# Optimization experiments

Hardware: AMD Instinct MI355X
Metric: run time of the kernel (lower is better)

Reference implementation:

```python
import jax, jax.numpy as jnp
import numpy as np
from jax import lax

T, B, D_IN, H, D_OUT = 512, 64, 256, 512, 256


def _lstm_scan(xs, h0, c0, Wih, Whh, b):
    """Standard LSTM over time. xs: [T,B,Din]; returns (hs [T,B,H], hT, cT).
    Gate order i,f,g,o (PyTorch convention)."""
    def step(carry, x_t):
        h, c = carry
        gates = x_t @ Wih.T + h @ Whh.T + b            # [B, 4H]
        i, f, g, o = jnp.split(gates, 4, axis=-1)
        i = jax.nn.sigmoid(i)
        f = jax.nn.sigmoid(f)
        g = jnp.tanh(g)
        o = jax.nn.sigmoid(o)
        c = f * c + i * g
        h = o * jnp.tanh(c)
        return (h, c), h
    (hT, cT), hs = lax.scan(step, (h0, c0), xs)
    return hs, hT, cT


def setup_inputs() -> dict:
    key = jax.random.key(0)
    ks = jax.random.split(key, 10)
    s = 0.05
    return {
        "x": jax.random.normal(ks[0], (T, B, D_IN), jnp.float32),
        "target": jax.random.uniform(ks[1], (T, B, D_OUT), jnp.float32),
        "hidden_state": jnp.zeros((1, B, H), jnp.float32),
        "cell_state": jnp.zeros((1, B, H), jnp.float32),
        "enc_Wih": jax.random.normal(ks[2], (4 * H, D_IN), jnp.float32) * s,
        "enc_Whh": jax.random.normal(ks[3], (4 * H, H), jnp.float32) * s,
        "enc_b": jax.random.normal(ks[4], (4 * H,), jnp.float32) * s,
        "dec_Wih": jax.random.normal(ks[5], (4 * H, D_OUT), jnp.float32) * s,
        "dec_Whh": jax.random.normal(ks[6], (4 * H, H), jnp.float32) * s,
        "dec_b": jax.random.normal(ks[7], (4 * H,), jnp.float32) * s,
        "fc_W": jax.random.normal(ks[8], (D_OUT, H), jnp.float32) * s,
        "fc_b": jax.random.normal(ks[9], (D_OUT,), jnp.float32) * s,
    }


def reference(x, target, hidden_state, cell_state,
              enc_Wih, enc_Whh, enc_b, dec_Wih, dec_Whh, dec_b, fc_W, fc_b):
    # Encoder: consume x, keep final (h, c).
    _, h, c = _lstm_scan(x, hidden_state[0], cell_state[0], enc_Wih, enc_Whh, enc_b)
    # Decoder with teacher_forcing = 1.0: input at step t is target[t-1],
    # step 0 input is zeros (matches torch code's initial x = zeros).
    dec_in = jnp.concatenate([jnp.zeros((1,) + target.shape[1:], target.dtype),
                              target[:-1]], axis=0)          # [T, B, D_OUT]
    hs, _, _ = _lstm_scan(dec_in, h, c, dec_Wih, dec_Whh, dec_b)  # [T, B, H]
    logits = hs @ fc_W.T + fc_b                                   # [T, B, D_OUT]
    return jax.nn.softmax(logits, axis=-1)
```

## Files before the change

### kernel.cpp

```cpp
#include <hip/hip_runtime.h>
#include <math.h>

#define TT 512
#define BB 64
#define DIN 256
#define HH 512
#define DOUT 256

#define RSU 388
#define RSH 776

#define W_HI_OFF 0
#define W_LO_OFF 12416
#define A_HI_OFF 24832
#define A_LO_OFF 31040
#define P_OFF    37248
#define B_OFF    38528
#define C_OFF    38560
#define HST_HI   38688
#define HST_LO   38752
#define SMEM_U32 38816
#define SMEM_BYTES (SMEM_U32*4)

#define FCS 516

typedef _Float16 f16x8 __attribute__((ext_vector_type(8)));
typedef float    f32x4 __attribute__((ext_vector_type(4)));
typedef unsigned u32x4 __attribute__((ext_vector_type(4)));

union H16 { _Float16 f; unsigned short u; };
__device__ __forceinline__ unsigned short f16bits(_Float16 h) { H16 t; t.f = h; return t.u; }

__device__ __forceinline__ void pack2(float x, float y, unsigned& hi, unsigned& lo) {
    _Float16 hx = (_Float16)x, hy = (_Float16)y;
    _Float16 lx = (_Float16)((x - (float)hx) * 2048.0f);
    _Float16 ly = (_Float16)((y - (float)hy) * 2048.0f);
    hi = (unsigned)f16bits(hx) | ((unsigned)f16bits(hy) << 16);
    lo = (unsigned)f16bits(lx) | ((unsigned)f16bits(ly) << 16);
}

__device__ __forceinline__ u32x4 ld16_cohere(const void* p) {
    u32x4 v;
    asm volatile("global_load_dwordx4 %0, %1, off sc0 sc1"
                 : "=&v"(v) : "v"(p) : "memory");
    return v;
}
__device__ __forceinline__ void st16_cohere(void* p, u32x4 v) {
    asm volatile("global_store_dwordx4 %0, %1, off sc0 sc1"
                 :: "v"(p), "v"(v) : "memory");
}

__device__ __forceinline__ void load_w_f16(unsigned* __restrict__ sm32, float* __restrict__ b_l,
                                           const float* __restrict__ Whh,
                                           const float* __restrict__ Wih,
                                           const float* __restrict__ bias,
                                           int u0, int tid) {
    for (int r = 0; r < 48; ++r) {
        int id = tid + 256*r;
        int cc = id / 384;
        int jj = id - cc*384;
        int C  = (cc >> 3)*HH + u0 + (cc & 7);
        float2 v;
        if (jj < 256) v = ((const float2*)(Whh + (size_t)C*HH))[jj];
        else          v = ((const float2*)(Wih + (size_t)C*DIN))[jj - 256];
        unsigned hi, lo;
        pack2(v.x, v.y, hi, lo);
        sm32[W_HI_OFF + cc*RSU + jj] = hi;
        sm32[W_LO_OFF + cc*RSU + jj] = lo;
    }
    if (tid < 32) {
        int C = (tid >> 3)*HH + u0 + (tid & 7);
        b_l[tid] = bias[C];
    }
}

__device__ __forceinline__ void stage_x_f16(unsigned* __restrict__ sm32,
                                            const float* __restrict__ src, int tid) {
    for (int r = 0; r < 4; ++r) {
        int idx4 = tid + 256*r;
        int b = idx4 >> 6, j4 = idx4 & 63;
        float4 v = ((const float4*)(src + (size_t)b*DIN))[j4];
        unsigned h0, l0, h1, l1;
        pack2(v.x, v.y, h0, l0);
        pack2(v.z, v.w, h1, l1);
        int o = b*RSU + 256 + 2*j4;
        sm32[A_HI_OFF + o]     = h0;
        sm32[A_HI_OFF + o + 1] = h1;
        sm32[A_LO_OFF + o]     = l0;
        sm32[A_LO_OFF + o + 1] = l1;
    }
}

__device__ __forceinline__ void stage_x_zero_f16(unsigned* __restrict__ sm32, int tid) {
    for (int r = 0; r < 4; ++r) {
        int idx4 = tid + 256*r;
        int b = idx4 >> 6, j4 = idx4 & 63;
        int o = b*RSU + 256 + 2*j4;
        sm32[A_HI_OFF + o]     = 0u;
        sm32[A_HI_OFF + o + 1] = 0u;
        sm32[A_LO_OFF + o]     = 0u;
        sm32[A_LO_OFF + o + 1] = 0u;
    }
}

__global__ __launch_bounds__(256, 1)
void lstm_persist(const float* __restrict__ x, const float* __restrict__ target,
                  const float* __restrict__ h0, const float* __restrict__ c0,
                  const float* __restrict__ eWih, const float* __restrict__ eWhh,
                  const float* __restrict__ eb,
                  const float* __restrict__ dWih, const float* __restrict__ dWhh,
                  const float* __restrict__ db,
                  float* __restrict__ hs,
                  unsigned short* __restrict__ hbh,
                  unsigned short* __restrict__ hbl,
                  unsigned* __restrict__ bar)
{
    extern __shared__ unsigned sm32[];
    float* p_l = (float*)(sm32 + P_OFF);
    float* b_l = (float*)(sm32 + B_OFF);
    float* c_l = (float*)(sm32 + C_OFF);
    unsigned* hst_hi = sm32 + HST_HI;
    unsigned* hst_lo = sm32 + HST_LO;

    const int tid = (int)threadIdx.x;
    const int xcd = (int)(blockIdx.x & 7);
    const int ib  = xcd >> 1;
    const int sub = xcd & 1;
    const int ij  = (int)(blockIdx.x >> 3) | (sub << 5);
    const int b0  = ib * 16;
    const int u0  = ij * 8;
    unsigned* gflags = bar + ib*64;

    load_w_f16(sm32, b_l, eWhh, eWih, eb, u0, tid);
    if (tid < 128) {
        int b = tid >> 3, u = tid & 7;
        c_l[tid] = c0[(size_t)(b0 + b)*HH + u0 + u];
    }
    stage_x_f16(sm32, x + (size_t)b0*DIN, tid);
    for (int r = 0; r < 8; ++r) {
        int idx4 = tid + 256*r;
        int b = idx4 >> 7, j4 = idx4 & 127;
        float4 v = ((const float4*)(h0 + (size_t)(b0 + b)*HH))[j4];
        unsigned h0p, l0p, h1p, l1p;
        pack2(v.x, v.y, h0p, l0p);
        pack2(v.z, v.w, h1p, l1p);
        int o = b*RSU + 2*j4;
        sm32[A_HI_OFF + o]     = h0p;
        sm32[A_HI_OFF + o + 1] = h1p;
        sm32[A_LO_OFF + o]     = l0p;
        sm32[A_LO_OFF + o + 1] = l1p;
    }
    __syncthreads();

    const int lane = tid & 63;
    const int wid  = tid >> 6;
    const int m    = lane & 15;
    const int q    = lane >> 4;
    const int ct   = wid & 1;
    const int kh   = wid >> 1;

    const _Float16* aH = (const _Float16*)(sm32 + A_HI_OFF);
    const _Float16* aL = (const _Float16*)(sm32 + A_LO_OFF);
    const _Float16* wH = (const _Float16*)(sm32 + W_HI_OFF);
    const _Float16* wL = (const _Float16*)(sm32 + W_LO_OFF);
    const int aoff = m*RSH + q*8;
    const int woff = (ct*16 + m)*RSH + q*8;

    for (int s = 0; s < 1024; ++s) {
        f32x4 Chh = {0.f, 0.f, 0.f, 0.f};
        f32x4 Chl = {0.f, 0.f, 0.f, 0.f};
        f32x4 Clh = {0.f, 0.f, 0.f, 0.f};
        {
            const int ks0 = kh * 12;
            #pragma unroll
            for (int i = 0; i < 12; ++i) {
                const int o = (ks0 + i) * 32;
                f16x8 ah = *(const f16x8*)(aH + aoff + o);
                f16x8 al = *(const f16x8*)(aL + aoff + o);
                f16x8 wh = *(const f16x8*)(wH + woff + o);
                f16x8 wl = *(const f16x8*)(wL + woff + o);
                Chh = __builtin_amdgcn_mfma_f32_16x16x32_f16(ah, wh, Chh, 0, 0, 0);
                Chl = __builtin_amdgcn_mfma_f32_16x16x32_f16(ah, wl, Chl, 0, 0, 0);
                Clh = __builtin_amdgcn_mfma_f32_16x16x32_f16(al, wh, Clh, 0, 0, 0);
            }
        }
        {
            float4 C;
            const float sc = 1.0f / 2048.0f;
            C.x = Chh[0] + (Chl[0] + Clh[0]) * sc;
            C.y = Chh[1] + (Chl[1] + Clh[1]) * sc;
            C.z = Chh[2] + (Chl[2] + Clh[2]) * sc;
            C.w = Chh[3] + (Chl[3] + Clh[3]) * sc;
            *(float4*)(p_l + (ct*2 + kh)*320 + m*20 + q*4) = C;
        }
        __syncthreads();

        float hval = 0.f;
        if (tid < 128) {
            int b = tid >> 3, u = tid & 7;
            float gi = p_l[      u*20 + b] + p_l[320 +      u*20 + b] + b_l[u];
            float gf = p_l[(8+u)*20 + b] + p_l[320 + (8+u)*20 + b] + b_l[8 + u];
            float gg = p_l[640 +   u*20 + b] + p_l[960 +      u*20 + b] + b_l[16 + u];
            float go = p_l[640 + (8+u)*20 + b] + p_l[960 + (8+u)*20 + b] + b_l[24 + u];
            float ii = 1.f / (1.f + expf(-gi));
            float ff = 1.f / (1.f + expf(-gf));
            float g2 = tanhf(gg);
            float oo = 1.f / (1.f + expf(-go));
            float c  = ff * c_l[tid] + ii * g2;
            c_l[tid] = c;
            hval = oo * tanhf(c);
            _Float16 hh = (_Float16)hval;
            _Float16 hl = (_Float16)((hval - (float)hh) * 2048.0f);
            ((unsigned short*)hst_hi)[tid] = f16bits(hh);
            ((unsigned short*)hst_lo)[tid] = f16bits(hl);
        }
        __syncthreads();

        if (tid < 64) {
            if (tid < 32) {
                int b    = tid & 15;
                int isLo = tid >> 4;
                u32x4 v = *(const u32x4*)((isLo ? hst_lo : hst_hi) + b*4);
                unsigned short* base = isLo ? hbl : hbh;
                st16_cohere(base + ((size_t)(((s & 1) ^ 1))*BB + b0 + b)*HH + u0, v);
            }
            asm volatile("s_waitcnt vmcnt(0)" ::: "memory");
            if (tid == 0)
                __hip_atomic_store(&gflags[ij], (unsigned)(s + 1),
                                   __ATOMIC_RELAXED, __HIP_MEMORY_SCOPE_AGENT);
        }

        if (s >= 512 && tid < 128) {
            int b = tid >> 3, u = tid & 7;
            hs[((size_t)(s - 512)*BB + (b0 + b))*HH + (u0 + u)] = hval;
        }
        if (s == 511) load_w_f16(sm32, b_l, dWhh, dWih, db, u0, tid);
        {
            int ns = s + 1;
            if (ns < 1024) {
                if (ns == 512)       stage_x_zero_f16(sm32, tid);
                else if (ns < 512)   stage_x_f16(sm32, x + ((size_t)ns*BB + b0)*DIN, tid);
                else                 stage_x_f16(sm32, target + ((size_t)(ns - 513)*BB + b0)*DOUT, tid);
            }
        }

        if (s < 1023) {
            if (tid < 64) {
                while (true) {
                    unsigned v = __hip_atomic_load(&gflags[tid], __ATOMIC_RELAXED,
                                                   __HIP_MEMORY_SCOPE_AGENT);
                    if (__ballot(v >= (unsigned)(s + 1)) == ~0ull) break;
                    __builtin_amdgcn_s_sleep(1);
                }
            }
            __syncthreads();
            const unsigned short* srcH = hbh + (size_t)((s + 1) & 1)*BB*HH + (size_t)b0*HH;
            const unsigned short* srcL = hbl + (size_t)((s + 1) & 1)*BB*HH + (size_t)b0*HH;
            u32x4 h0v = ld16_cohere((const u32x4*)srcH + tid);
            u32x4 h1v = ld16_cohere((const u32x4*)srcH + tid + 256);
            u32x4 h2v = ld16_cohere((const u32x4*)srcH + tid + 512);
            u32x4 h3v = ld16_cohere((const u32x4*)srcH + tid + 768);
            u32x4 l0v = ld16_cohere((const u32x4*)srcL + tid);
            u32x4 l1v = ld16_cohere((const u32x4*)srcL + tid + 256);
            u32x4 l2v = ld16_cohere((const u32x4*)srcL + tid + 512);
            u32x4 l3v = ld16_cohere((const u32x4*)srcL + tid + 768);
            asm volatile("s_waitcnt vmcnt(0)"
                         : "+v"(h0v), "+v"(h1v), "+v"(h2v), "+v"(h3v),
                           "+v"(l0v), "+v"(l1v), "+v"(l2v), "+v"(l3v) :: "memory");
            {
                int idx, b, j0;
                idx = tid;       b = idx >> 6; j0 = (idx & 63)*4;
                *(u32x4*)(sm32 + A_HI_OFF + b*RSU + j0) = h0v;
                *(u32x4*)(sm32 + A_LO_OFF + b*RSU + j0) = l0v;
                idx = tid + 256; b = idx >> 6; j0 = (idx & 63)*4;
                *(u32x4*)(sm32 + A_HI_OFF + b*RSU + j0) = h1v;
                *(u32x4*)(sm32 + A_LO_OFF + b*RSU + j0) = l1v;
                idx = tid + 512; b = idx >> 6; j0 = (idx & 63)*4;
                *(u32x4*)(sm32 + A_HI_OFF + b*RSU + j0) = h2v;
                *(u32x4*)(sm32 + A_LO_OFF + b*RSU + j0) = l2v;
                idx = tid + 768; b = idx >> 6; j0 = (idx & 63)*4;
                *(u32x4*)(sm32 + A_HI_OFF + b*RSU + j0) = h3v;
                *(u32x4*)(sm32 + A_LO_OFF + b*RSU + j0) = l3v;
            }
        }
        __syncthreads();
    }
}

__global__ __launch_bounds__(256, 1)
void fc_kernel(const float* __restrict__ hs, const float* __restrict__ W,
               const float* __restrict__ bias, float* __restrict__ out)
{
    extern __shared__ float sm[];
    float* hs_l = sm;
    float* w_l  = sm + 16*FCS;

    const int tid = (int)threadIdx.x;
    const int rb = (int)(blockIdx.x >> 3);
    const int cb = (int)(blockIdx.x & 7);

    for (int r = 0; r < 8; ++r) {
        int id = tid + 256*r;
        int b = id >> 7, j = id & 127;
        float4 v = ((const float4*)(hs + (size_t)(rb*16 + b)*HH))[j];
        *(float4*)(hs_l + b*FCS + 4*j) = v;
    }
    for (int r = 0; r < 16; ++r) {
        int id = tid + 256*r;
        int c = id >> 7, j = id & 127;
        float4 v = ((const float4*)(W + (size_t)(cb*32 + c)*HH))[j];
        *(float4*)(w_l + c*FCS + 4*j) = v;
    }
    __syncthreads();

    const int kc = tid & 7, bt = (tid >> 3) & 3, ct = tid >> 5;
    float acc[4][4] = {};
    const float* ap = hs_l + (bt*4)*FCS + 4*kc;
    const float* wp = w_l  + (ct*4)*FCS + 4*kc;
    #pragma unroll 4
    for (int i = 0; i < 16; ++i) {
        float4 av[4], wv[4];
        #pragma unroll
        for (int q = 0; q < 4; ++q) av[q] = *(const float4*)(ap + q*FCS + 32*i);
        #pragma unroll
        for (int q = 0; q < 4; ++q) wv[q] = *(const float4*)(wp + q*FCS + 32*i);
        #pragma unroll
        for (int b2 = 0; b2 < 4; ++b2)
            #pragma unroll
            for (int c2 = 0; c2 < 4; ++c2)
                acc[b2][c2] += av[b2].x*wv[c2].x + av[b2].y*wv[c2].y
                             + av[b2].z*wv[c2].z + av[b2].w*wv[c2].w;
    }
    #pragma unroll
    for (int b2 = 0; b2 < 4; ++b2)
        #pragma unroll
        for (int c2 = 0; c2 < 4; ++c2) {
            float v = acc[b2][c2];
            v += __shfl_xor(v, 1, 64);
            v += __shfl_xor(v, 2, 64);
            v += __shfl_xor(v, 4, 64);
            acc[b2][c2] = v;
        }
    if (kc == 0) {
        #pragma unroll
        for (int b2 = 0; b2 < 4; ++b2)
            #pragma unroll
            for (int c2 = 0; c2 < 4; ++c2) {
                int row = rb*16 + bt*4 + b2;
                int col = cb*32 + ct*4 + c2;
                out[(size_t)row*DOUT + col] = acc[b2][c2] + bias[col];
            }
    }
}

__global__ __launch_bounds__(256, 1)
void softmax_kernel(float* __restrict__ out)
{
    int row  = (int)blockIdx.x * 4 + ((int)threadIdx.x >> 6);
    int lane = (int)threadIdx.x & 63;
    float4 v = ((const float4*)(out + (size_t)row*DOUT))[lane];
    float m = fmaxf(fmaxf(v.x, v.y), fmaxf(v.z, v.w));
    #pragma unroll
    for (int d = 1; d < 64; d <<= 1) m = fmaxf(m, __shfl_xor(m, d, 64));
    float ex = expf(v.x - m), ey = expf(v.y - m), ez = expf(v.z - m), ew = expf(v.w - m);
    float ssum = ex + ey + ez + ew;
    #pragma unroll
    for (int d = 1; d < 64; d <<= 1) ssum += __shfl_xor(ssum, d, 64);
    float inv = 1.f / ssum;
    float4 o = make_float4(ex*inv, ey*inv, ez*inv, ew*inv);
    ((float4*)(out + (size_t)row*DOUT))[lane] = o;
}

__global__ void init_kernel(unsigned* __restrict__ bar)
{
    bar[threadIdx.x] = 0u;
}

extern "C" void kernel_launch(void* const* d_in, const int* in_sizes, int n_in,
                              void* d_out, int out_size, void* d_ws, size_t ws_size,
                              hipStream_t stream) {
    (void)in_sizes; (void)n_in; (void)out_size; (void)ws_size;
    const float* x      = (const float*)d_in[0];
    const float* target = (const float*)d_in[1];
    const float* h0     = (const float*)d_in[2];
    const float* c0     = (const float*)d_in[3];
    const float* eWih   = (const float*)d_in[4];
    const float* eWhh   = (const float*)d_in[5];
    const float* eb     = (const float*)d_in[6];
    const float* dWih   = (const float*)d_in[7];
    const float* dWhh   = (const float*)d_in[8];
    const float* db     = (const float*)d_in[9];
    const float* fcW    = (const float*)d_in[10];
    const float* fcb    = (const float*)d_in[11];
    float* out = (float*)d_out;

    unsigned* bar = (unsigned*)d_ws;
    float* hs = (float*)d_ws + 1024;
    unsigned short* hbh = (unsigned short*)(hs + (size_t)TT*BB*HH);
    unsigned short* hbl = hbh + (size_t)2*BB*HH;

    init_kernel<<<dim3(1), dim3(1024), 0, stream>>>(bar);

    lstm_persist<<<dim3(256), dim3(256), SMEM_BYTES, stream>>>(
        x, target, h0, c0, eWih, eWhh, eb, dWih, dWhh, db, hs, hbh, hbl, bar);

    size_t lds_fc = (size_t)(48*FCS) * sizeof(float);
    fc_kernel<<<dim3(16384), dim3(256), lds_fc, stream>>>(hs, fcW, fcb, out);

    softmax_kernel<<<dim3(8192), dim3(256), 0, stream>>>(out);
}
```

Before: 4.658 ms.

## Precompute input projection off critical path and reorder hidden-state exchange layout

The input-side MFMA products (x·Wih) for the next step are now computed right after the current step finishes, before the barrier wait. This takes them off the serialized critical path, so the in-loop matmul only covers the recurrent h·Whh part. The global hidden-state exchange buffer is laid out per batch-group in a contiguous block, so each block writes one contiguous chunk and reads contiguously. Staging of the next input and writing of hs are moved onto otherwise idle threads. These changes add accumulator registers and make the staging and indexing logic more intricate.

```diff
diff --git a/kernel.cpp b/kernel.cpp
--- a/kernel.cpp
+++ b/kernel.cpp
@@ -30,6 +30,7 @@
 
 union H16 { _Float16 f; unsigned short u; };
 __device__ __forceinline__ unsigned short f16bits(_Float16 h) { H16 t; t.f = h; return t.u; }
+__device__ __forceinline__ float f16val(unsigned short b) { H16 t; t.u = b; return (float)t.f; }
 
 __device__ __forceinline__ void pack2(float x, float y, unsigned& hi, unsigned& lo) {
     _Float16 hx = (_Float16)x, hy = (_Float16)y;
@@ -71,35 +72,6 @@
     if (tid < 32) {
         int C = (tid >> 3)*HH + u0 + (tid & 7);
         b_l[tid] = bias[C];
-    }
-}
-
-__device__ __forceinline__ void stage_x_f16(unsigned* __restrict__ sm32,
-                                            const float* __restrict__ src, int tid) {
-    for (int r = 0; r < 4; ++r) {
-        int idx4 = tid + 256*r;
-        int b = idx4 >> 6, j4 = idx4 & 63;
-        float4 v = ((const float4*)(src + (size_t)b*DIN))[j4];
-        unsigned h0, l0, h1, l1;
-        pack2(v.x, v.y, h0, l0);
-        pack2(v.z, v.w, h1, l1);
-        int o = b*RSU + 256 + 2*j4;
-        sm32[A_HI_OFF + o]     = h0;
-        sm32[A_HI_OFF + o + 1] = h1;
-        sm32[A_LO_OFF + o]     = l0;
-        sm32[A_LO_OFF + o + 1] = l1;
-    }
-}
-
-__device__ __forceinline__ void stage_x_zero_f16(unsigned* __restrict__ sm32, int tid) {
-    for (int r = 0; r < 4; ++r) {
-        int idx4 = tid + 256*r;
-        int b = idx4 >> 6, j4 = idx4 & 63;
-        int o = b*RSU + 256 + 2*j4;
-        sm32[A_HI_OFF + o]     = 0u;
-        sm32[A_HI_OFF + o + 1] = 0u;
-        sm32[A_LO_OFF + o]     = 0u;
-        sm32[A_LO_OFF + o + 1] = 0u;
     }
 }
 
@@ -136,19 +108,31 @@
         int b = tid >> 3, u = tid & 7;
         c_l[tid] = c0[(size_t)(b0 + b)*HH + u0 + u];
     }
-    stage_x_f16(sm32, x + (size_t)b0*DIN, tid);
+    for (int r = 0; r < 4; ++r) {
+        int idx4 = tid + 256*r;
+        int b = idx4 >> 6, j4 = idx4 & 63;
+        float4 v = ((const float4*)(x + ((size_t)b0 + b)*DIN))[j4];
+        unsigned hp0, lp0, hp1, lp1;
+        pack2(v.x, v.y, hp0, lp0);
+        pack2(v.z, v.w, hp1, lp1);
+        int o = b*RSU + 256 + 2*j4;
+        sm32[A_HI_OFF + o]     = hp0;
+        sm32[A_HI_OFF + o + 1] = hp1;
+        sm32[A_LO_OFF + o]     = lp0;
+        sm32[A_LO_OFF + o + 1] = lp1;
+    }
     for (int r = 0; r < 8; ++r) {
         int idx4 = tid + 256*r;
         int b = idx4 >> 7, j4 = idx4 & 127;
         float4 v = ((const float4*)(h0 + (size_t)(b0 + b)*HH))[j4];
-        unsigned h0p, l0p, h1p, l1p;
-        pack2(v.x, v.y, h0p, l0p);
-        pack2(v.z, v.w, h1p, l1p);
+        unsigned hp0, lp0, hp1, lp1;
+        pack2(v.x, v.y, hp0, lp0);
+        pack2(v.z, v.w, hp1, lp1);
         int o = b*RSU + 2*j4;
-        sm32[A_HI_OFF + o]     = h0p;
-        sm32[A_HI_OFF + o + 1] = h1p;
-        sm32[A_LO_OFF + o]     = l0p;
-        sm32[A_LO_OFF + o + 1] = l1p;
+        sm32[A_HI_OFF + o]     = hp0;
+        sm32[A_HI_OFF + o + 1] = hp1;
+        sm32[A_LO_OFF + o]     = lp0;
+        sm32[A_LO_OFF + o + 1] = lp1;
     }
     __syncthreads();
 
@@ -166,15 +150,71 @@
     const int aoff = m*RSH + q*8;
     const int woff = (ct*16 + m)*RSH + q*8;
 
+    f32x4 Ahh = {0.f,0.f,0.f,0.f}, Ahl = {0.f,0.f,0.f,0.f}, Alh = {0.f,0.f,0.f,0.f};
+    {
+        const int xs0 = 16 + kh*4;
+        #pragma unroll
+        for (int i = 0; i < 4; ++i) {
+            const int o = (xs0 + i) * 32;
+            f16x8 ah = *(const f16x8*)(aH + aoff + o);
+            f16x8 al = *(const f16x8*)(aL + aoff + o);
+            f16x8 wh = *(const f16x8*)(wH + woff + o);
+            f16x8 wl = *(const f16x8*)(wL + woff + o);
+            Ahh = __builtin_amdgcn_mfma_f32_16x16x32_f16(ah, wh, Ahh, 0, 0, 0);
+            Ahl = __builtin_amdgcn_mfma_f32_16x16x32_f16(ah, wl, Ahl, 0, 0, 0);
+            Alh = __builtin_amdgcn_mfma_f32_16x16x32_f16(al, wh, Alh, 0, 0, 0);
+        }
+    }
+
     for (int s = 0; s < 1024; ++s) {
-        f32x4 Chh = {0.f, 0.f, 0.f, 0.f};
-        f32x4 Chl = {0.f, 0.f, 0.f, 0.f};
-        f32x4 Clh = {0.f, 0.f, 0.f, 0.f};
+        if (s > 0) {
+            if (tid < 64) {
+                while (true) {
+                    unsigned v = __hip_atomic_load(&gflags[tid], __ATOMIC_RELAXED,
+                                                   __HIP_MEMORY_SCOPE_AGENT);
+                    if (__ballot(v >= (unsigned)s) == ~0ull) break;
+                    __builtin_amdgcn_s_sleep(1);
+                }
+            }
+            __syncthreads();
+            const int buf = s & 1;
+            const unsigned short* srcH = hbh + ((size_t)ib*2 + buf)*8192;
+            const unsigned short* srcL = hbl + ((size_t)ib*2 + buf)*8192;
+            u32x4 hv0 = ld16_cohere((const u32x4*)srcH + tid);
+            u32x4 hv1 = ld16_cohere((const u32x4*)srcH + tid + 256);
+            u32x4 hv2 = ld16_cohere((const u32x4*)srcH + tid + 512);
+            u32x4 hv3 = ld16_cohere((const u32x4*)srcH + tid + 768);
+            u32x4 lv0 = ld16_cohere((const u32x4*)srcL + tid);
+            u32x4 lv1 = ld16_cohere((const u32x4*)srcL + tid + 256);
+            u32x4 lv2 = ld16_cohere((const u32x4*)srcL + tid + 512);
+            u32x4 lv3 = ld16_cohere((const u32x4*)srcL + tid + 768);
+            asm volatile("s_waitcnt vmcnt(0)"
+                         : "+v"(hv0), "+v"(hv1), "+v"(hv2), "+v"(hv3),
+                           "+v"(lv0), "+v"(lv1), "+v"(lv2), "+v"(lv3) :: "memory");
+            {
+                int c, b, jp;
+                c = tid;       b = c & 15; jp = c >> 4;
+                *(u32x4*)(sm32 + A_HI_OFF + b*RSU + jp*4) = hv0;
+                *(u32x4*)(sm32 + A_LO_OFF + b*RSU + jp*4) = lv0;
+                c = tid + 256; b = c & 15; jp = c >> 4;
+                *(u32x4*)(sm32 + A_HI_OFF + b*RSU + jp*4) = hv1;
+                *(u32x4*)(sm32 + A_LO_OFF + b*RSU + jp*4) = lv1;
+                c = tid + 512; b = c & 15; jp = c >> 4;
+                *(u32x4*)(sm32 + A_HI_OFF + b*RSU + jp*4) = hv2;
+                *(u32x4*)(sm32 + A_LO_OFF + b*RSU + jp*4) = lv2;
+                c = tid + 768; b = c & 15; jp = c >> 4;
+                *(u32x4*)(sm32 + A_HI_OFF + b*RSU + jp*4) = hv3;
+                *(u32x4*)(sm32 + A_LO_OFF + b*RSU + jp*4) = lv3;
+            }
+            __syncthreads();
+        }
+
+        f32x4 Chh = Ahh, Chl = Ahl, Clh = Alh;
         {
-            const int ks0 = kh * 12;
+            const int hs0 = kh * 8;
             #pragma unroll
-            for (int i = 0; i < 12; ++i) {
-                const int o = (ks0 + i) * 32;
+            for (int i = 0; i < 8; ++i) {
+                const int o = (hs0 + i) * 32;
                 f16x8 ah = *(const f16x8*)(aH + aoff + o);
                 f16x8 al = *(const f16x8*)(aL + aoff + o);
                 f16x8 wh = *(const f16x8*)(wH + woff + o);
@@ -195,7 +235,6 @@
         }
         __syncthreads();
 
-        float hval = 0.f;
         if (tid < 128) {
             int b = tid >> 3, u = tid & 7;
             float gi = p_l[      u*20 + b] + p_l[320 +      u*20 + b] + b_l[u];
@@ -208,7 +247,7 @@
             float oo = 1.f / (1.f + expf(-go));
             float c  = ff * c_l[tid] + ii * g2;
             c_l[tid] = c;
-            hval = oo * tanhf(c);
+            float hval = oo * tanhf(c);
             _Float16 hh = (_Float16)hval;
             _Float16 hl = (_Float16)((hval - (float)hh) * 2048.0f);
             ((unsigned short*)hst_hi)[tid] = f16bits(hh);
@@ -216,74 +255,86 @@
         }
         __syncthreads();
 
+        const int ns = s + 1;
+
         if (tid < 64) {
+            const int nbuf = (s & 1) ^ 1;
             if (tid < 32) {
-                int b    = tid & 15;
-                int isLo = tid >> 4;
-                u32x4 v = *(const u32x4*)((isLo ? hst_lo : hst_hi) + b*4);
-                unsigned short* base = isLo ? hbl : hbh;
-                st16_cohere(base + ((size_t)(((s & 1) ^ 1))*BB + b0 + b)*HH + u0, v);
+                unsigned short* dst = (tid < 16)
+                    ? hbh + ((size_t)ib*2 + nbuf)*8192 + (size_t)ij*128 + (tid & 15)*8
+                    : hbl + ((size_t)ib*2 + nbuf)*8192 + (size_t)ij*128 + (tid & 15)*8;
+                u32x4 v = (tid < 16) ? *(const u32x4*)(hst_hi + (tid & 15)*4)
+                                     : *(const u32x4*)(hst_lo + (tid & 15)*4);
+                st16_cohere(dst, v);
             }
             asm volatile("s_waitcnt vmcnt(0)" ::: "memory");
             if (tid == 0)
-                __hip_atomic_store(&gflags[ij], (unsigned)(s + 1),
+                __hip_atomic_store(&gflags[ij], (unsigned)ns,
                                    __ATOMIC_RELAXED, __HIP_MEMORY_SCOPE_AGENT);
         }
 
-        if (s >= 512 && tid < 128) {
-            int b = tid >> 3, u = tid & 7;
-            hs[((size_t)(s - 512)*BB + (b0 + b))*HH + (u0 + u)] = hval;
-        }
+        if (tid >= 64 && ns < 1024) {
+            int t = tid - 64;
+            if (ns == 512) {
+                for (int r = 0; r < 6; ++r) {
+                    int idx4 = t + 192*r;
+                    if (idx4 < 1024) {
+                        int b = idx4 >> 6, j4 = idx4 & 63;
+                        int o = b*RSU + 256 + 2*j4;
+                        sm32[A_HI_OFF + o]     = 0u;
+                        sm32[A_HI_OFF + o + 1] = 0u;
+                        sm32[A_LO_OFF + o]     = 0u;
+                        sm32[A_LO_OFF + o + 1] = 0u;
+                    }
+                }
+            } else {
+                const float* src = (ns < 512) ? x + ((size_t)ns*BB + b0)*DIN
+                                              : target + ((size_t)(ns - 513)*BB + b0)*DOUT;
+                for (int r = 0; r < 6; ++r) {
+                    int idx4 = t + 192*r;
+                    if (idx4 < 1024) {
+                        int b = idx4 >> 6, j4 = idx4 & 63;
+                        float4 v = ((const float4*)(src + (size_t)b*DIN))[j4];
+                        unsigned hp0, lp0, hp1, lp1;
+                        pack2(v.x, v.y, hp0, lp0);
+                        pack2(v.z, v.w, hp1, lp1);
+                        int o = b*RSU + 256 + 2*j4;
+                        sm32[A_HI_OFF + o]     = hp0;
+                        sm32[A_HI_OFF + o + 1] = hp1;
+                        sm32[A_LO_OFF + o]     = lp0;
+                        sm32[A_LO_OFF + o + 1] = lp1;
+                    }
+                }
+            }
+        }
+
+        if (tid >= 128 && s >= 512) {
+            int t = tid - 128;
+            int b = t >> 3, u = t & 7;
+            float h = f16val(((unsigned short*)hst_hi)[t])
+                    + f16val(((unsigned short*)hst_lo)[t]) * (1.0f/2048.0f);
+            hs[((size_t)(s - 512)*BB + (b0 + b))*HH + (u0 + u)] = h;
+        }
+
         if (s == 511) load_w_f16(sm32, b_l, dWhh, dWih, db, u0, tid);
-        {
-            int ns = s + 1;
-            if (ns < 1024) {
-                if (ns == 512)       stage_x_zero_f16(sm32, tid);
-                else if (ns < 512)   stage_x_f16(sm32, x + ((size_t)ns*BB + b0)*DIN, tid);
-                else                 stage_x_f16(sm32, target + ((size_t)(ns - 513)*BB + b0)*DOUT, tid);
-            }
-        }
-
-        if (s < 1023) {
-            if (tid < 64) {
-                while (true) {
-                    unsigned v = __hip_atomic_load(&gflags[tid], __ATOMIC_RELAXED,
-                                                   __HIP_MEMORY_SCOPE_AGENT);
-                    if (__ballot(v >= (unsigned)(s + 1)) == ~0ull) break;
-                    __builtin_amdgcn_s_sleep(1);
-                }
-            }
-            __syncthreads();
-            const unsigned short* srcH = hbh + (size_t)((s + 1) & 1)*BB*HH + (size_t)b0*HH;
-            const unsigned short* srcL = hbl + (size_t)((s + 1) & 1)*BB*HH + (size_t)b0*HH;
-            u32x4 h0v = ld16_cohere((const u32x4*)srcH + tid);
-            u32x4 h1v = ld16_cohere((const u32x4*)srcH + tid + 256);
-            u32x4 h2v = ld16_cohere((const u32x4*)srcH + tid + 512);
-            u32x4 h3v = ld16_cohere((const u32x4*)srcH + tid + 768);
-            u32x4 l0v = ld16_cohere((const u32x4*)srcL + tid);
-            u32x4 l1v = ld16_cohere((const u32x4*)srcL + tid + 256);
-            u32x4 l2v = ld16_cohere((const u32x4*)srcL + tid + 512);
-            u32x4 l3v = ld16_cohere((const u32x4*)srcL + tid + 768);
-            asm volatile("s_waitcnt vmcnt(0)"
-                         : "+v"(h0v), "+v"(h1v), "+v"(h2v), "+v"(h3v),
-                           "+v"(l0v), "+v"(l1v), "+v"(l2v), "+v"(l3v) :: "memory");
-            {
-                int idx, b, j0;
-                idx = tid;       b = idx >> 6; j0 = (idx & 63)*4;
-                *(u32x4*)(sm32 + A_HI_OFF + b*RSU + j0) = h0v;
-                *(u32x4*)(sm32 + A_LO_OFF + b*RSU + j0) = l0v;
-                idx = tid + 256; b = idx >> 6; j0 = (idx & 63)*4;
-                *(u32x4*)(sm32 + A_HI_OFF + b*RSU + j0) = h1v;
-                *(u32x4*)(sm32 + A_LO_OFF + b*RSU + j0) = l1v;
-                idx = tid + 512; b = idx >> 6; j0 = (idx & 63)*4;
-                *(u32x4*)(sm32 + A_HI_OFF + b*RSU + j0) = h2v;
-                *(u32x4*)(sm32 + A_LO_OFF + b*RSU + j0) = l2v;
-                idx = tid + 768; b = idx >> 6; j0 = (idx & 63)*4;
-                *(u32x4*)(sm32 + A_HI_OFF + b*RSU + j0) = h3v;
-                *(u32x4*)(sm32 + A_LO_OFF + b*RSU + j0) = l3v;
-            }
-        }
         __syncthreads();
+
+        if (ns < 1024) {
+            f32x4 Xhh = {0.f,0.f,0.f,0.f}, Xhl = {0.f,0.f,0.f,0.f}, Xlh = {0.f,0.f,0.f,0.f};
+            const int xs0 = 16 + kh*4;
+            #pragma unroll
+            for (int i = 0; i < 4; ++i) {
+                const int o = (xs0 + i) * 32;
+                f16x8 ah = *(const f16x8*)(aH + aoff + o);
+                f16x8 al = *(const f16x8*)(aL + aoff + o);
+                f16x8 wh = *(const f16x8*)(wH + woff + o);
+                f16x8 wl = *(const f16x8*)(wL + woff + o);
+                Xhh = __builtin_amdgcn_mfma_f32_16x16x32_f16(ah, wh, Xhh, 0, 0, 0);
+                Xhl = __builtin_amdgcn_mfma_f32_16x16x32_f16(ah, wl, Xhl, 0, 0, 0);
+                Xlh = __builtin_amdgcn_mfma_f32_16x16x32_f16(al, wh, Xlh, 0, 0, 0);
+            }
+            Ahh = Xhh; Ahl = Xhl; Alh = Xlh;
+        }
     }
 }
 
@@ -397,7 +448,7 @@
     unsigned* bar = (unsigned*)d_ws;
     float* hs = (float*)d_ws + 1024;
     unsigned short* hbh = (unsigned short*)(hs + (size_t)TT*BB*HH);
-    unsigned short* hbl = hbh + (size_t)2*BB*HH;
+    unsigned short* hbl = hbh + (size_t)4*2*8192;
 
     init_kernel<<<dim3(1), dim3(1024), 0, stream>>>(bar);
 
```

After: 5.712 ms. +22.6%, slower.
